# Optimization experiments

Hardware: AMD Instinct MI355X
Metric: run time of the kernel (lower is better)

Reference implementation:

```python
import jax, jax.numpy as jnp
import numpy as np

N = 50000      # nodes
E = 800000     # edges (avg degree 16)
D = 64         # hidden_dim = heads * per-head channels
H = 4          # heads
C = D // H     # per-head channels
EDIM = 16      # edge feature dim
L = 3          # num_layers
NEG_SLOPE = 0.2


def setup_inputs() -> dict:
    key = jax.random.key(0)
    ks = jax.random.split(key, 11)
    s = 0.1
    return {
        "x": jax.random.normal(ks[0], (N, D), dtype=jnp.float32),
        "edge_index": jax.random.randint(ks[1], (2, E), 0, N, dtype=jnp.int32),
        "edge_attr": jax.random.normal(ks[2], (E, EDIM), dtype=jnp.float32),
        # stacked per-layer GATv2 parameters (all layers have in=out=D)
        "Wl": jax.random.normal(ks[3], (L, D, D), dtype=jnp.float32) * s,
        "bl": jnp.zeros((L, D), dtype=jnp.float32),
        "Wr": jax.random.normal(ks[4], (L, D, D), dtype=jnp.float32) * s,
        "br": jnp.zeros((L, D), dtype=jnp.float32),
        "We": jax.random.normal(ks[5], (L, EDIM, D), dtype=jnp.float32) * s,
        "att": jax.random.normal(ks[6], (L, H, C), dtype=jnp.float32) * s,
        "bias": jnp.zeros((L, D), dtype=jnp.float32),
    }


def _gatv2_layer(x, src, dst, edge_attr, Wl, bl, Wr, br, We, att, bias):
    # x: [N, D] -> out: [N, D] (concat of H heads of C channels)
    xl = (x @ Wl + bl).reshape(N, H, C)          # source transform (message value)
    xr = (x @ Wr + br).reshape(N, H, C)          # target transform
    ef = (edge_attr @ We).reshape(E, H, C)       # edge feature transform
    m = jax.nn.leaky_relu(xl[src] + xr[dst] + ef, NEG_SLOPE)  # [E, H, C]
    score = jnp.einsum('ehc,hc->eh', m, att)     # [E, H]
    # segment softmax over incoming edges of each target node
    smax = jax.ops.segment_max(score, dst, num_segments=N)   # [N, H]
    ex = jnp.exp(score - smax[dst])                          # [E, H]
    denom = jax.ops.segment_sum(ex, dst, num_segments=N)     # [N, H]
    alpha = ex / denom[dst]                                  # [E, H]
    out = jax.ops.segment_sum(alpha[:, :, None] * xl[src], dst, num_segments=N)
    return out.reshape(N, D) + bias


def reference(x, edge_index, edge_attr, Wl, bl, Wr, br, We, att, bias):
    src, dst = edge_index[0], edge_index[1]
    h = x
    for l in range(L):
        h = _gatv2_layer(h, src, dst, edge_attr,
                         Wl[l], bl[l], Wr[l], br[l], We[l], att[l], bias[l])
        h = jax.nn.relu(h)
    return h
```

## Files before the change

### kernel.cpp

```cpp
#include <hip/hip_runtime.h>
#include <cfloat>

#define NEG_SLOPE 0.2f

__global__ __launch_bounds__(256) void zero_kernel(int* __restrict__ counts,
                                                   int* __restrict__ cursor, int n) {
    int gid = blockIdx.x * 256 + threadIdx.x;
    if (gid < n) { counts[gid] = 0; cursor[gid] = 0; }
}

__global__ __launch_bounds__(256) void count_kernel(const int* __restrict__ dst,
                                                    int* __restrict__ counts, int E) {
    int e = blockIdx.x * 256 + threadIdx.x;
    if (e < E) atomicAdd(&counts[dst[e]], 1);
}

__global__ __launch_bounds__(256) void scan_bsums_kernel(const int* __restrict__ counts,
                                                         int* __restrict__ bsums, int N) {
    int t = threadIdx.x;
    int base = blockIdx.x * 1024 + t * 4;
    int s = 0;
    #pragma unroll
    for (int i = 0; i < 4; ++i) { int idx = base + i; if (idx < N) s += counts[idx]; }
    #pragma unroll
    for (int d = 1; d < 64; d <<= 1) s += __shfl_xor(s, d);
    __shared__ int ws[4];
    if ((t & 63) == 0) ws[t >> 6] = s;
    __syncthreads();
    if (t == 0) bsums[blockIdx.x] = ws[0] + ws[1] + ws[2] + ws[3];
}

__global__ __launch_bounds__(64) void scan_bscan_kernel(int* __restrict__ bsums, int NB) {
    int t = threadIdx.x;
    int v = (t < NB) ? bsums[t] : 0;
    int x = v;
    #pragma unroll
    for (int d = 1; d < 64; d <<= 1) {
        int y = __shfl_up(x, d);
        if (t >= d) x += y;
    }
    if (t < NB) bsums[t] = x - v;
}

__global__ __launch_bounds__(256) void scan_final_kernel(const int* __restrict__ counts,
                                                         const int* __restrict__ bsums,
                                                         int* __restrict__ offs, int N) {
    int t = threadIdx.x, lane = t & 63, w = t >> 6;
    int base = blockIdx.x * 1024 + t * 4;
    int v[4]; int s = 0;
    #pragma unroll
    for (int i = 0; i < 4; ++i) { int idx = base + i; v[i] = (idx < N) ? counts[idx] : 0; s += v[i]; }
    int x = s;
    #pragma unroll
    for (int d = 1; d < 64; d <<= 1) {
        int y = __shfl_up(x, d);
        if (lane >= d) x += y;
    }
    __shared__ int wtot[4];
    if (lane == 63) wtot[w] = x;
    __syncthreads();
    int wexc = 0;
    for (int i = 0; i < w; ++i) wexc += wtot[i];
    int run = (x - s) + wexc + bsums[blockIdx.x];
    #pragma unroll
    for (int i = 0; i < 4; ++i) {
        int idx = base + i;
        run += v[i];
        if (idx < N) offs[idx + 1] = run;
    }
    if (blockIdx.x == 0 && t == 0) offs[0] = 0;
}

__global__ __launch_bounds__(256) void scatter_kernel(
    const int* __restrict__ src, const int* __restrict__ dst,
    const int* __restrict__ offs, int* __restrict__ cursor,
    int* __restrict__ csr_src, int* __restrict__ csr_dst,
    int* __restrict__ csr_eid, int E) {
    int e = blockIdx.x * 256 + threadIdx.x;
    if (e >= E) return;
    int d = dst[e];
    int pos = offs[d] + atomicAdd(&cursor[d], 1);
    csr_src[pos] = src[e];
    csr_dst[pos] = d;
    csr_eid[pos] = e;
}

__global__ __launch_bounds__(256) void sort_segments_kernel(
    int* __restrict__ csr_src, int* __restrict__ csr_eid,
    const int* __restrict__ offs, int N)
{
    int t = threadIdx.x;
    int lane = t & 63;
    int node = blockIdx.x * 4 + (t >> 6);
    if (node >= N) return;
    int off = offs[node];
    int deg = offs[node + 1] - off;
    if (deg <= 1) return;
    if (deg <= 64) {
        int key = 0x7FFFFFFF, val = 0;
        if (lane < deg) { key = csr_eid[off + lane]; val = csr_src[off + lane]; }
        int rank = 0;
        #pragma unroll
        for (int i = 0; i < 64; ++i) {
            int ki = __shfl(key, i);
            if (ki < key) rank++;
        }
        if (lane < deg) { csr_eid[off + rank] = key; csr_src[off + rank] = val; }
    } else if (lane == 0) {
        for (int a = 1; a < deg; ++a) {
            int k = csr_eid[off + a], v = csr_src[off + a];
            int b = a - 1;
            while (b >= 0 && csr_eid[off + b] > k) {
                csr_eid[off + b + 1] = csr_eid[off + b];
                csr_src[off + b + 1] = csr_src[off + b];
                b--;
            }
            csr_eid[off + b + 1] = k;
            csr_src[off + b + 1] = v;
        }
    }
}

#define XSTRIDE 68
__global__ __launch_bounds__(256) void node_gemm_kernel(
    const float* __restrict__ hin,
    const float* __restrict__ Wl, const float* __restrict__ bl,
    const float* __restrict__ Wr, const float* __restrict__ br,
    float* __restrict__ xl, float* __restrict__ xr, int nrows)
{
    __shared__ float sWl[4096];
    __shared__ float sWr[4096];
    __shared__ float sX[64 * XSTRIDE];
    int t = threadIdx.x;
    {
        float4* dl = (float4*)sWl; const float4* sl = (const float4*)Wl;
        float4* dr = (float4*)sWr; const float4* sr = (const float4*)Wr;
        for (int i = t; i < 1024; i += 256) { dl[i] = sl[i]; dr[i] = sr[i]; }
    }
    int row0 = blockIdx.x * 64;
    for (int i = t; i < 1024; i += 256) {
        int rr = i >> 4;
        int cc = (i & 15) << 2;
        int row = row0 + rr;
        float4 v = make_float4(0.f, 0.f, 0.f, 0.f);
        if (row < nrows) v = *(const float4*)(hin + (size_t)row * 64 + cc);
        *(float4*)(&sX[rr * XSTRIDE + cc]) = v;
    }
    __syncthreads();

    int lane = t & 63;
    int w = t >> 6;
    int rs = lane >> 4;
    int c4 = lane & 15;
    float4 bl4 = *(const float4*)(bl + c4 * 4);
    float4 br4 = *(const float4*)(br + c4 * 4);

    #pragma unroll
    for (int g = 0; g < 4; ++g) {
        int rloc = w * 16 + g * 4 + rs;
        int row = row0 + rloc;
        float4 al = {0.f, 0.f, 0.f, 0.f};
        float4 ar = {0.f, 0.f, 0.f, 0.f};
        const float* xrow = &sX[rloc * XSTRIDE];
        #pragma unroll 4
        for (int k = 0; k < 64; ++k) {
            float xk = xrow[k];
            float4 wl4 = *(const float4*)(&sWl[k * 64 + c4 * 4]);
            float4 wr4 = *(const float4*)(&sWr[k * 64 + c4 * 4]);
            al.x += xk * wl4.x; al.y += xk * wl4.y;
            al.z += xk * wl4.z; al.w += xk * wl4.w;
            ar.x += xk * wr4.x; ar.y += xk * wr4.y;
            ar.z += xk * wr4.z; ar.w += xk * wr4.w;
        }
        if (row < nrows) {
            float4 ol, orr;
            ol.x = al.x + bl4.x; ol.y = al.y + bl4.y;
            ol.z = al.z + bl4.z; ol.w = al.w + bl4.w;
            orr.x = ar.x + br4.x; orr.y = ar.y + br4.y;
            orr.z = ar.z + br4.z; orr.w = ar.w + br4.w;
            *(float4*)(xl + (size_t)row * 64 + c4 * 4) = ol;
            *(float4*)(xr + (size_t)row * 64 + c4 * 4) = orr;
        }
    }
}

__global__ __launch_bounds__(256) void edge_score_kernel(
    const float* __restrict__ xl, const float* __restrict__ xr,
    const float* __restrict__ ea,
    const int* __restrict__ csr_src, const int* __restrict__ csr_dst,
    const int* __restrict__ csr_eid,
    const float* __restrict__ We, const float* __restrict__ att,
    float* __restrict__ score_csr, int E)
{
    __shared__ float sWe[1024];
    __shared__ float sAtt[64];
    int t = threadIdx.x;
    for (int i = t; i < 1024; i += 256) sWe[i] = We[i];
    if (t < 64) sAtt[t] = att[t];
    __syncthreads();
    int gid = blockIdx.x * 256 + t;
    int pos = gid >> 2, h = gid & 3;
    if (pos >= E) return;
    int s = csr_src[pos], d = csr_dst[pos], eid = csr_eid[pos];
    const float4* eap = (const float4*)(ea + (size_t)eid * 16);
    float4 a0 = eap[0], a1 = eap[1], a2 = eap[2], a3 = eap[3];
    float av[16] = {a0.x, a0.y, a0.z, a0.w, a1.x, a1.y, a1.z, a1.w,
                    a2.x, a2.y, a2.z, a2.w, a3.x, a3.y, a3.z, a3.w};
    const float4* xls = (const float4*)(xl + (size_t)s * 64 + h * 16);
    const float4* xrd = (const float4*)(xr + (size_t)d * 64 + h * 16);
    float4 vl0 = xls[0], vl1 = xls[1], vl2 = xls[2], vl3 = xls[3];
    float4 vr0 = xrd[0], vr1 = xrd[1], vr2 = xrd[2], vr3 = xrd[3];

    float ef[16];
    #pragma unroll
    for (int c = 0; c < 16; ++c) ef[c] = 0.f;
    #pragma unroll
    for (int k = 0; k < 16; ++k) {
        float a = av[k];
        const float* wrow = &sWe[k * 64 + h * 16];
        #pragma unroll
        for (int c = 0; c < 16; ++c) ef[c] += a * wrow[c];
    }

    float lv[16] = {vl0.x, vl0.y, vl0.z, vl0.w, vl1.x, vl1.y, vl1.z, vl1.w,
                    vl2.x, vl2.y, vl2.z, vl2.w, vl3.x, vl3.y, vl3.z, vl3.w};
    float rv[16] = {vr0.x, vr0.y, vr0.z, vr0.w, vr1.x, vr1.y, vr1.z, vr1.w,
                    vr2.x, vr2.y, vr2.z, vr2.w, vr3.x, vr3.y, vr3.z, vr3.w};
    float sc0 = 0.f, sc1 = 0.f, sc2 = 0.f, sc3 = 0.f;
    #pragma unroll
    for (int c = 0; c < 16; c += 4) {
        float m0 = lv[c] + rv[c] + ef[c];
        float m1 = lv[c+1] + rv[c+1] + ef[c+1];
        float m2 = lv[c+2] + rv[c+2] + ef[c+2];
        float m3 = lv[c+3] + rv[c+3] + ef[c+3];
        m0 = (m0 >= 0.f) ? m0 : NEG_SLOPE * m0;
        m1 = (m1 >= 0.f) ? m1 : NEG_SLOPE * m1;
        m2 = (m2 >= 0.f) ? m2 : NEG_SLOPE * m2;
        m3 = (m3 >= 0.f) ? m3 : NEG_SLOPE * m3;
        sc0 += m0 * sAtt[h * 16 + c];
        sc1 += m1 * sAtt[h * 16 + c + 1];
        sc2 += m2 * sAtt[h * 16 + c + 2];
        sc3 += m3 * sAtt[h * 16 + c + 3];
    }
    score_csr[gid] = (sc0 + sc1) + (sc2 + sc3);
}

__global__ __launch_bounds__(256) void node_pass_kernel(
    const float* __restrict__ score_csr, const float* __restrict__ xl,
    const int* __restrict__ csr_src,
    const int* __restrict__ offs, const float* __restrict__ bias,
    float* __restrict__ hout, int N)
{
    int t = threadIdx.x;
    int lane = t & 63;
    int node = blockIdx.x * 4 + (t >> 6);
    if (node >= N) return;
    int eg = lane >> 4;
    int k  = lane & 15;
    int h  = k >> 2;
    int off = offs[node];
    int deg = offs[node + 1] - off;

    if (deg == 0) {
        if (eg == 0) {
            float4 b = *(const float4*)(bias + k * 4);
            float4 o;
            o.x = fmaxf(b.x, 0.f); o.y = fmaxf(b.y, 0.f);
            o.z = fmaxf(b.z, 0.f); o.w = fmaxf(b.w, 0.f);
            *(float4*)(hout + (size_t)node * 64 + k * 4) = o;
        }
        return;
    }

    float mx = -FLT_MAX;
    for (int j0 = 0; j0 < deg; j0 += 4) {
        int j = j0 + eg;
        if (j < deg) {
            float sc = score_csr[(size_t)(off + j) * 4 + h];
            mx = fmaxf(mx, sc);
        }
    }
    mx = fmaxf(mx, __shfl_xor(mx, 16));
    mx = fmaxf(mx, __shfl_xor(mx, 32));

    float4 acc = {0.f, 0.f, 0.f, 0.f};
    float sSum = 0.f;
    for (int j0 = 0; j0 < deg; j0 += 4) {
        int j = j0 + eg;
        int jj = (j < deg) ? j : deg - 1;
        int pos = off + jj;
        int s = csr_src[pos];
        float sc = score_csr[(size_t)pos * 4 + h];
        float ex = (j < deg) ? __expf(sc - mx) : 0.f;
        float4 v = *(const float4*)(xl + (size_t)s * 64 + k * 4);
        acc.x += ex * v.x; acc.y += ex * v.y;
        acc.z += ex * v.z; acc.w += ex * v.w;
        sSum += ex;
    }

    acc.x += __shfl_xor(acc.x, 16); acc.y += __shfl_xor(acc.y, 16);
    acc.z += __shfl_xor(acc.z, 16); acc.w += __shfl_xor(acc.w, 16);
    sSum  += __shfl_xor(sSum, 16);
    acc.x += __shfl_xor(acc.x, 32); acc.y += __shfl_xor(acc.y, 32);
    acc.z += __shfl_xor(acc.z, 32); acc.w += __shfl_xor(acc.w, 32);
    sSum  += __shfl_xor(sSum, 32);

    if (eg == 0) {
        float inv = 1.f / sSum;
        float4 b = *(const float4*)(bias + k * 4);
        float4 o;
        o.x = fmaxf(acc.x * inv + b.x, 0.f);
        o.y = fmaxf(acc.y * inv + b.y, 0.f);
        o.z = fmaxf(acc.z * inv + b.z, 0.f);
        o.w = fmaxf(acc.w * inv + b.w, 0.f);
        *(float4*)(hout + (size_t)node * 64 + k * 4) = o;
    }
}

extern "C" void kernel_launch(void* const* d_in, const int* in_sizes, int n_in,
                              void* d_out, int out_size, void* d_ws, size_t ws_size,
                              hipStream_t stream) {
    const float* x    = (const float*)d_in[0];
    const int*   eidx = (const int*)d_in[1];
    const float* ea   = (const float*)d_in[2];
    const float* Wl   = (const float*)d_in[3];
    const float* bl   = (const float*)d_in[4];
    const float* Wr   = (const float*)d_in[5];
    const float* br   = (const float*)d_in[6];
    const float* We   = (const float*)d_in[7];
    const float* att  = (const float*)d_in[8];
    const float* bias = (const float*)d_in[9];
    float* out = (float*)d_out;

    const int N = in_sizes[0] / 64;
    const int E = in_sizes[1] / 2;
    const int* src = eidx;
    const int* dst = eidx + E;

    float* ws = (float*)d_ws;
    float* xl      = ws;
    float* xr      = xl + (size_t)N * 64;
    float* score   = xr + (size_t)N * 64;
    float* h_tmp   = score + (size_t)E * 4;
    int* counts    = (int*)(h_tmp + (size_t)N * 64);
    int* cursor    = counts + N;
    int* offs      = cursor + N;
    int* csr_src   = offs + N + 1;
    int* csr_dst   = csr_src + E;
    int* csr_eid   = csr_dst + E;
    int* bsums     = csr_eid + E;

    dim3 blk(256);
    int g_n    = (N + 255) / 256;
    int g_e    = (E + 255) / 256;
    int g_eh   = (E * 4 + 255) / 256;
    int g_gemm = (N + 63) / 64;
    int g_node = (N + 3) / 4;
    int NB     = (N + 1023) / 1024;

    zero_kernel<<<g_n, blk, 0, stream>>>(counts, cursor, N);
    count_kernel<<<g_e, blk, 0, stream>>>(dst, counts, E);
    scan_bsums_kernel<<<NB, blk, 0, stream>>>(counts, bsums, N);
    scan_bscan_kernel<<<1, 64, 0, stream>>>(bsums, NB);
    scan_final_kernel<<<NB, blk, 0, stream>>>(counts, bsums, offs, N);
    scatter_kernel<<<g_e, blk, 0, stream>>>(src, dst, offs, cursor,
                                            csr_src, csr_dst, csr_eid, E);
    sort_segments_kernel<<<g_node, blk, 0, stream>>>(csr_src, csr_eid, offs, N);

    const float* hin = x;
    for (int l = 0; l < 3; ++l) {
        float* hout = (l == 2) ? out : h_tmp;
        node_gemm_kernel<<<g_gemm, blk, 0, stream>>>(hin, Wl + (size_t)l * 4096, bl + l * 64,
                                                     Wr + (size_t)l * 4096, br + l * 64, xl, xr, N);
        edge_score_kernel<<<g_eh, blk, 0, stream>>>(xl, xr, ea, csr_src, csr_dst, csr_eid,
                                                    We + (size_t)l * 1024, att + l * 64,
                                                    score, E);
        node_pass_kernel<<<g_node, blk, 0, stream>>>(score, xl, csr_src, offs,
                                                     bias + l * 64, hout, N);
        hin = hout;
    }
}
```

Baseline: 512.5 us.

## Fuse edge scoring and softmax aggregation into one online-softmax node kernel

Replaces the separate per-edge score kernel and per-node softmax/aggregation kernel with a single kernel in which each wavefront handles one destination node. It computes edge features, scores and an online softmax over incoming edges, so the score buffer is never written or read back. It also packs the CSR src and edge-id arrays into one int2 array and drops csr_dst. The trade-off is a serial per-edge loop within each wavefront, with a shuffle reduction and exp calls on every edge, which gives less parallelism than the old edge-parallel scoring.

Measured after the change: 625.9 us. +22.1%, slower.

```diff
diff --git a/kernel.cpp b/kernel.cpp
--- a/kernel.cpp
+++ b/kernel.cpp
@@ -74,20 +74,16 @@
 __global__ __launch_bounds__(256) void scatter_kernel(
     const int* __restrict__ src, const int* __restrict__ dst,
     const int* __restrict__ offs, int* __restrict__ cursor,
-    int* __restrict__ csr_src, int* __restrict__ csr_dst,
-    int* __restrict__ csr_eid, int E) {
+    int2* __restrict__ csr_se, int E) {
     int e = blockIdx.x * 256 + threadIdx.x;
     if (e >= E) return;
     int d = dst[e];
     int pos = offs[d] + atomicAdd(&cursor[d], 1);
-    csr_src[pos] = src[e];
-    csr_dst[pos] = d;
-    csr_eid[pos] = e;
+    csr_se[pos] = make_int2(src[e], e);
 }
 
 __global__ __launch_bounds__(256) void sort_segments_kernel(
-    int* __restrict__ csr_src, int* __restrict__ csr_eid,
-    const int* __restrict__ offs, int N)
+    int2* __restrict__ csr_se, const int* __restrict__ offs, int N)
 {
     int t = threadIdx.x;
     int lane = t & 63;
@@ -98,25 +94,23 @@
     if (deg <= 1) return;
     if (deg <= 64) {
         int key = 0x7FFFFFFF, val = 0;
-        if (lane < deg) { key = csr_eid[off + lane]; val = csr_src[off + lane]; }
+        if (lane < deg) { int2 se = csr_se[off + lane]; key = se.y; val = se.x; }
         int rank = 0;
         #pragma unroll
         for (int i = 0; i < 64; ++i) {
             int ki = __shfl(key, i);
             if (ki < key) rank++;
         }
-        if (lane < deg) { csr_eid[off + rank] = key; csr_src[off + rank] = val; }
+        if (lane < deg) csr_se[off + rank] = make_int2(val, key);
     } else if (lane == 0) {
         for (int a = 1; a < deg; ++a) {
-            int k = csr_eid[off + a], v = csr_src[off + a];
+            int2 kv = csr_se[off + a];
             int b = a - 1;
-            while (b >= 0 && csr_eid[off + b] > k) {
-                csr_eid[off + b + 1] = csr_eid[off + b];
-                csr_src[off + b + 1] = csr_src[off + b];
+            while (b >= 0 && csr_se[off + b].y > kv.y) {
+                csr_se[off + b + 1] = csr_se[off + b];
                 b--;
             }
-            csr_eid[off + b + 1] = k;
-            csr_src[off + b + 1] = v;
+            csr_se[off + b + 1] = kv;
         }
     }
 }
@@ -184,137 +178,56 @@
     }
 }
 
-__global__ __launch_bounds__(256) void edge_score_kernel(
+__global__ __launch_bounds__(256) void fused_attn_kernel(
     const float* __restrict__ xl, const float* __restrict__ xr,
     const float* __restrict__ ea,
-    const int* __restrict__ csr_src, const int* __restrict__ csr_dst,
-    const int* __restrict__ csr_eid,
+    const int2* __restrict__ csr_se, const int* __restrict__ offs,
     const float* __restrict__ We, const float* __restrict__ att,
-    float* __restrict__ score_csr, int E)
-{
-    __shared__ float sWe[1024];
-    __shared__ float sAtt[64];
-    int t = threadIdx.x;
-    for (int i = t; i < 1024; i += 256) sWe[i] = We[i];
-    if (t < 64) sAtt[t] = att[t];
-    __syncthreads();
-    int gid = blockIdx.x * 256 + t;
-    int pos = gid >> 2, h = gid & 3;
-    if (pos >= E) return;
-    int s = csr_src[pos], d = csr_dst[pos], eid = csr_eid[pos];
-    const float4* eap = (const float4*)(ea + (size_t)eid * 16);
-    float4 a0 = eap[0], a1 = eap[1], a2 = eap[2], a3 = eap[3];
-    float av[16] = {a0.x, a0.y, a0.z, a0.w, a1.x, a1.y, a1.z, a1.w,
-                    a2.x, a2.y, a2.z, a2.w, a3.x, a3.y, a3.z, a3.w};
-    const float4* xls = (const float4*)(xl + (size_t)s * 64 + h * 16);
-    const float4* xrd = (const float4*)(xr + (size_t)d * 64 + h * 16);
-    float4 vl0 = xls[0], vl1 = xls[1], vl2 = xls[2], vl3 = xls[3];
-    float4 vr0 = xrd[0], vr1 = xrd[1], vr2 = xrd[2], vr3 = xrd[3];
-
-    float ef[16];
-    #pragma unroll
-    for (int c = 0; c < 16; ++c) ef[c] = 0.f;
-    #pragma unroll
-    for (int k = 0; k < 16; ++k) {
-        float a = av[k];
-        const float* wrow = &sWe[k * 64 + h * 16];
-        #pragma unroll
-        for (int c = 0; c < 16; ++c) ef[c] += a * wrow[c];
-    }
-
-    float lv[16] = {vl0.x, vl0.y, vl0.z, vl0.w, vl1.x, vl1.y, vl1.z, vl1.w,
-                    vl2.x, vl2.y, vl2.z, vl2.w, vl3.x, vl3.y, vl3.z, vl3.w};
-    float rv[16] = {vr0.x, vr0.y, vr0.z, vr0.w, vr1.x, vr1.y, vr1.z, vr1.w,
-                    vr2.x, vr2.y, vr2.z, vr2.w, vr3.x, vr3.y, vr3.z, vr3.w};
-    float sc0 = 0.f, sc1 = 0.f, sc2 = 0.f, sc3 = 0.f;
-    #pragma unroll
-    for (int c = 0; c < 16; c += 4) {
-        float m0 = lv[c] + rv[c] + ef[c];
-        float m1 = lv[c+1] + rv[c+1] + ef[c+1];
-        float m2 = lv[c+2] + rv[c+2] + ef[c+2];
-        float m3 = lv[c+3] + rv[c+3] + ef[c+3];
-        m0 = (m0 >= 0.f) ? m0 : NEG_SLOPE * m0;
-        m1 = (m1 >= 0.f) ? m1 : NEG_SLOPE * m1;
-        m2 = (m2 >= 0.f) ? m2 : NEG_SLOPE * m2;
-        m3 = (m3 >= 0.f) ? m3 : NEG_SLOPE * m3;
-        sc0 += m0 * sAtt[h * 16 + c];
-        sc1 += m1 * sAtt[h * 16 + c + 1];
-        sc2 += m2 * sAtt[h * 16 + c + 2];
-        sc3 += m3 * sAtt[h * 16 + c + 3];
-    }
-    score_csr[gid] = (sc0 + sc1) + (sc2 + sc3);
-}
-
-__global__ __launch_bounds__(256) void node_pass_kernel(
-    const float* __restrict__ score_csr, const float* __restrict__ xl,
-    const int* __restrict__ csr_src,
-    const int* __restrict__ offs, const float* __restrict__ bias,
-    float* __restrict__ hout, int N)
+    const float* __restrict__ bias, float* __restrict__ hout, int N)
 {
     int t = threadIdx.x;
     int lane = t & 63;
     int node = blockIdx.x * 4 + (t >> 6);
     if (node >= N) return;
-    int eg = lane >> 4;
-    int k  = lane & 15;
-    int h  = k >> 2;
+
+    float wv[16];
+    #pragma unroll
+    for (int k = 0; k < 16; ++k) wv[k] = We[k * 64 + lane];
+    float attc = att[lane];
+    float bc   = bias[lane];
+    float xrc  = xr[(size_t)node * 64 + lane];
+
     int off = offs[node];
     int deg = offs[node + 1] - off;
 
-    if (deg == 0) {
-        if (eg == 0) {
-            float4 b = *(const float4*)(bias + k * 4);
-            float4 o;
-            o.x = fmaxf(b.x, 0.f); o.y = fmaxf(b.y, 0.f);
-            o.z = fmaxf(b.z, 0.f); o.w = fmaxf(b.w, 0.f);
-            *(float4*)(hout + (size_t)node * 64 + k * 4) = o;
-        }
-        return;
-    }
-
-    float mx = -FLT_MAX;
-    for (int j0 = 0; j0 < deg; j0 += 4) {
-        int j = j0 + eg;
-        if (j < deg) {
-            float sc = score_csr[(size_t)(off + j) * 4 + h];
-            mx = fmaxf(mx, sc);
-        }
-    }
-    mx = fmaxf(mx, __shfl_xor(mx, 16));
-    mx = fmaxf(mx, __shfl_xor(mx, 32));
-
-    float4 acc = {0.f, 0.f, 0.f, 0.f};
-    float sSum = 0.f;
-    for (int j0 = 0; j0 < deg; j0 += 4) {
-        int j = j0 + eg;
-        int jj = (j < deg) ? j : deg - 1;
-        int pos = off + jj;
-        int s = csr_src[pos];
-        float sc = score_csr[(size_t)pos * 4 + h];
-        float ex = (j < deg) ? __expf(sc - mx) : 0.f;
-        float4 v = *(const float4*)(xl + (size_t)s * 64 + k * 4);
-        acc.x += ex * v.x; acc.y += ex * v.y;
-        acc.z += ex * v.z; acc.w += ex * v.w;
-        sSum += ex;
-    }
-
-    acc.x += __shfl_xor(acc.x, 16); acc.y += __shfl_xor(acc.y, 16);
-    acc.z += __shfl_xor(acc.z, 16); acc.w += __shfl_xor(acc.w, 16);
-    sSum  += __shfl_xor(sSum, 16);
-    acc.x += __shfl_xor(acc.x, 32); acc.y += __shfl_xor(acc.y, 32);
-    acc.z += __shfl_xor(acc.z, 32); acc.w += __shfl_xor(acc.w, 32);
-    sSum  += __shfl_xor(sSum, 32);
-
-    if (eg == 0) {
-        float inv = 1.f / sSum;
-        float4 b = *(const float4*)(bias + k * 4);
-        float4 o;
-        o.x = fmaxf(acc.x * inv + b.x, 0.f);
-        o.y = fmaxf(acc.y * inv + b.y, 0.f);
-        o.z = fmaxf(acc.z * inv + b.z, 0.f);
-        o.w = fmaxf(acc.w * inv + b.w, 0.f);
-        *(float4*)(hout + (size_t)node * 64 + k * 4) = o;
-    }
+    float m = -FLT_MAX, s = 0.f, acc = 0.f;
+    for (int j = 0; j < deg; ++j) {
+        int2 se = csr_se[off + j];
+        const float4* ap = (const float4*)(ea + (size_t)se.y * 16);
+        float4 a0 = ap[0], a1 = ap[1], a2 = ap[2], a3 = ap[3];
+        float xlc = xl[(size_t)se.x * 64 + lane];
+        float ef = a0.x * wv[0]  + a0.y * wv[1]  + a0.z * wv[2]  + a0.w * wv[3]
+                 + a1.x * wv[4]  + a1.y * wv[5]  + a1.z * wv[6]  + a1.w * wv[7]
+                 + a2.x * wv[8]  + a2.y * wv[9]  + a2.z * wv[10] + a2.w * wv[11]
+                 + a3.x * wv[12] + a3.y * wv[13] + a3.z * wv[14] + a3.w * wv[15];
+        float mm = xlc + xrc + ef;
+        mm = (mm >= 0.f) ? mm : NEG_SLOPE * mm;
+        float sc = mm * attc;
+        sc += __shfl_xor(sc, 1);
+        sc += __shfl_xor(sc, 2);
+        sc += __shfl_xor(sc, 4);
+        sc += __shfl_xor(sc, 8);
+        float nm = fmaxf(m, sc);
+        float scale = __expf(m - nm);
+        float p = __expf(sc - nm);
+        s   = s * scale + p;
+        acc = acc * scale + p * xlc;
+        m = nm;
+    }
+
+    float v = (deg > 0) ? (acc / s) : 0.f;
+    v += bc;
+    hout[(size_t)node * 64 + lane] = fmaxf(v, 0.f);
 }
 
 extern "C" void kernel_launch(void* const* d_in, const int* in_sizes, int n_in,
@@ -340,20 +253,16 @@
     float* ws = (float*)d_ws;
     float* xl      = ws;
     float* xr      = xl + (size_t)N * 64;
-    float* score   = xr + (size_t)N * 64;
-    float* h_tmp   = score + (size_t)E * 4;
+    float* h_tmp   = xr + (size_t)N * 64;
     int* counts    = (int*)(h_tmp + (size_t)N * 64);
     int* cursor    = counts + N;
     int* offs      = cursor + N;
-    int* csr_src   = offs + N + 1;
-    int* csr_dst   = csr_src + E;
-    int* csr_eid   = csr_dst + E;
-    int* bsums     = csr_eid + E;
+    int* bsums     = offs + N + 1;
+    int2* csr_se   = (int2*)(bsums + 64);
 
     dim3 blk(256);
     int g_n    = (N + 255) / 256;
     int g_e    = (E + 255) / 256;
-    int g_eh   = (E * 4 + 255) / 256;
     int g_gemm = (N + 63) / 64;
     int g_node = (N + 3) / 4;
     int NB     = (N + 1023) / 1024;
@@ -363,20 +272,17 @@
     scan_bsums_kernel<<<NB, blk, 0, stream>>>(counts, bsums, N);
     scan_bscan_kernel<<<1, 64, 0, stream>>>(bsums, NB);
     scan_final_kernel<<<NB, blk, 0, stream>>>(counts, bsums, offs, N);
-    scatter_kernel<<<g_e, blk, 0, stream>>>(src, dst, offs, cursor,
-                                            csr_src, csr_dst, csr_eid, E);
-    sort_segments_kernel<<<g_node, blk, 0, stream>>>(csr_src, csr_eid, offs, N);
+    scatter_kernel<<<g_e, blk, 0, stream>>>(src, dst, offs, cursor, csr_se, E);
+    sort_segments_kernel<<<g_node, blk, 0, stream>>>(csr_se, offs, N);
 
     const float* hin = x;
     for (int l = 0; l < 3; ++l) {
         float* hout = (l == 2) ? out : h_tmp;
         node_gemm_kernel<<<g_gemm, blk, 0, stream>>>(hin, Wl + (size_t)l * 4096, bl + l * 64,
                                                      Wr + (size_t)l * 4096, br + l * 64, xl, xr, N);
-        edge_score_kernel<<<g_eh, blk, 0, stream>>>(xl, xr, ea, csr_src, csr_dst, csr_eid,
-                                                    We + (size_t)l * 1024, att + l * 64,
-                                                    score, E);
-        node_pass_kernel<<<g_node, blk, 0, stream>>>(score, xl, csr_src, offs,
-                                                     bias + l * 64, hout, N);
+        fused_attn_kernel<<<g_node, blk, 0, stream>>>(xl, xr, ea, csr_se, offs,
+                                                      We + (size_t)l * 1024, att + l * 64,
+                                                      bias + l * 64, hout, N);
         hin = hout;
     }
 }
```

## Pack CSR edge arrays into int4 and pre-permute edge attributes into CSR order

Applied to the files above, without the earlier changes.

Merges the separate src, dst and edge-id CSR arrays into one int4 array per edge, so each edge's indices are fetched with a single 16-byte load. Adds a one-time kernel that copies edge_attr into CSR order, so the three per-layer edge-score passes read edge features contiguously instead of gathering them by edge id. The permuted copy is used only when the workspace is large enough; otherwise the code falls back to the gather. The cost is an extra 51 MB copy pass and a larger CSR footprint (padding lane), and node_pass now loads a 16-byte struct where it previously loaded a 4-byte int.

Result: slower. 527.1 us (+2.9%).

```diff
diff --git a/kernel.cpp b/kernel.cpp
--- a/kernel.cpp
+++ b/kernel.cpp
@@ -74,20 +74,16 @@
 __global__ __launch_bounds__(256) void scatter_kernel(
     const int* __restrict__ src, const int* __restrict__ dst,
     const int* __restrict__ offs, int* __restrict__ cursor,
-    int* __restrict__ csr_src, int* __restrict__ csr_dst,
-    int* __restrict__ csr_eid, int E) {
+    int4* __restrict__ csr, int E) {
     int e = blockIdx.x * 256 + threadIdx.x;
     if (e >= E) return;
     int d = dst[e];
     int pos = offs[d] + atomicAdd(&cursor[d], 1);
-    csr_src[pos] = src[e];
-    csr_dst[pos] = d;
-    csr_eid[pos] = e;
+    csr[pos] = make_int4(src[e], d, e, 0);
 }
 
 __global__ __launch_bounds__(256) void sort_segments_kernel(
-    int* __restrict__ csr_src, int* __restrict__ csr_eid,
-    const int* __restrict__ offs, int N)
+    int4* __restrict__ csr, const int* __restrict__ offs, int N)
 {
     int t = threadIdx.x;
     int lane = t & 63;
@@ -97,28 +93,38 @@
     int deg = offs[node + 1] - off;
     if (deg <= 1) return;
     if (deg <= 64) {
-        int key = 0x7FFFFFFF, val = 0;
-        if (lane < deg) { key = csr_eid[off + lane]; val = csr_src[off + lane]; }
+        int key = 0x7FFFFFFF; int4 kv = make_int4(0, 0, 0, 0);
+        if (lane < deg) { kv = csr[off + lane]; key = kv.z; }
         int rank = 0;
         #pragma unroll
         for (int i = 0; i < 64; ++i) {
             int ki = __shfl(key, i);
             if (ki < key) rank++;
         }
-        if (lane < deg) { csr_eid[off + rank] = key; csr_src[off + rank] = val; }
+        if (lane < deg) csr[off + rank] = kv;
     } else if (lane == 0) {
         for (int a = 1; a < deg; ++a) {
-            int k = csr_eid[off + a], v = csr_src[off + a];
+            int4 kv = csr[off + a];
             int b = a - 1;
-            while (b >= 0 && csr_eid[off + b] > k) {
-                csr_eid[off + b + 1] = csr_eid[off + b];
-                csr_src[off + b + 1] = csr_src[off + b];
+            while (b >= 0 && csr[off + b].z > kv.z) {
+                csr[off + b + 1] = csr[off + b];
                 b--;
             }
-            csr_eid[off + b + 1] = k;
-            csr_src[off + b + 1] = v;
-        }
-    }
+            csr[off + b + 1] = kv;
+        }
+    }
+}
+
+__global__ __launch_bounds__(256) void eaperm_kernel(
+    const float* __restrict__ ea, const int4* __restrict__ csr,
+    float* __restrict__ eaperm, int E)
+{
+    int gid = blockIdx.x * 256 + threadIdx.x;
+    int pos = gid >> 2, q = gid & 3;
+    if (pos >= E) return;
+    int eid = csr[pos].z;
+    *(float4*)(eaperm + (size_t)pos * 16 + q * 4) =
+        *(const float4*)(ea + (size_t)eid * 16 + q * 4);
 }
 
 #define XSTRIDE 68
@@ -186,9 +192,8 @@
 
 __global__ __launch_bounds__(256) void edge_score_kernel(
     const float* __restrict__ xl, const float* __restrict__ xr,
-    const float* __restrict__ ea,
-    const int* __restrict__ csr_src, const int* __restrict__ csr_dst,
-    const int* __restrict__ csr_eid,
+    const float* __restrict__ ea, const float* __restrict__ eaperm, int use_perm,
+    const int4* __restrict__ csr,
     const float* __restrict__ We, const float* __restrict__ att,
     float* __restrict__ score_csr, int E)
 {
@@ -201,8 +206,11 @@
     int gid = blockIdx.x * 256 + t;
     int pos = gid >> 2, h = gid & 3;
     if (pos >= E) return;
-    int s = csr_src[pos], d = csr_dst[pos], eid = csr_eid[pos];
-    const float4* eap = (const float4*)(ea + (size_t)eid * 16);
+    int4 se = csr[pos];
+    int s = se.x, d = se.y;
+    const float4* eap = use_perm
+        ? (const float4*)(eaperm + (size_t)pos * 16)
+        : (const float4*)(ea + (size_t)se.z * 16);
     float4 a0 = eap[0], a1 = eap[1], a2 = eap[2], a3 = eap[3];
     float av[16] = {a0.x, a0.y, a0.z, a0.w, a1.x, a1.y, a1.z, a1.w,
                     a2.x, a2.y, a2.z, a2.w, a3.x, a3.y, a3.z, a3.w};
@@ -247,7 +255,7 @@
 
 __global__ __launch_bounds__(256) void node_pass_kernel(
     const float* __restrict__ score_csr, const float* __restrict__ xl,
-    const int* __restrict__ csr_src,
+    const int4* __restrict__ csr,
     const int* __restrict__ offs, const float* __restrict__ bias,
     float* __restrict__ hout, int N)
 {
@@ -289,7 +297,7 @@
         int j = j0 + eg;
         int jj = (j < deg) ? j : deg - 1;
         int pos = off + jj;
-        int s = csr_src[pos];
+        int s = csr[pos].x;
         float sc = score_csr[(size_t)pos * 4 + h];
         float ex = (j < deg) ? __expf(sc - mx) : 0.f;
         float4 v = *(const float4*)(xl + (size_t)s * 64 + k * 4);
@@ -345,10 +353,15 @@
     int* counts    = (int*)(h_tmp + (size_t)N * 64);
     int* cursor    = counts + N;
     int* offs      = cursor + N;
-    int* csr_src   = offs + N + 1;
-    int* csr_dst   = csr_src + E;
-    int* csr_eid   = csr_dst + E;
-    int* bsums     = csr_eid + E;
+    int* bsums     = offs + N + 1;
+    uintptr_t p    = (uintptr_t)(bsums + 64);
+    p = (p + 15) & ~(uintptr_t)15;
+    int4* csr      = (int4*)p;
+    float* eaperm  = (float*)(csr + E);
+
+    size_t need_base = (uintptr_t)(eaperm) - (uintptr_t)d_ws;
+    size_t need_perm = need_base + (size_t)E * 16 * sizeof(float);
+    int use_perm = (ws_size >= need_perm) ? 1 : 0;
 
     dim3 blk(256);
     int g_n    = (N + 255) / 256;
@@ -363,19 +376,20 @@
     scan_bsums_kernel<<<NB, blk, 0, stream>>>(counts, bsums, N);
     scan_bscan_kernel<<<1, 64, 0, stream>>>(bsums, NB);
     scan_final_kernel<<<NB, blk, 0, stream>>>(counts, bsums, offs, N);
-    scatter_kernel<<<g_e, blk, 0, stream>>>(src, dst, offs, cursor,
-                                            csr_src, csr_dst, csr_eid, E);
-    sort_segments_kernel<<<g_node, blk, 0, stream>>>(csr_src, csr_eid, offs, N);
+    scatter_kernel<<<g_e, blk, 0, stream>>>(src, dst, offs, cursor, csr, E);
+    sort_segments_kernel<<<g_node, blk, 0, stream>>>(csr, offs, N);
+    if (use_perm)
+        eaperm_kernel<<<g_eh, blk, 0, stream>>>(ea, csr, eaperm, E);
 
     const float* hin = x;
     for (int l = 0; l < 3; ++l) {
         float* hout = (l == 2) ? out : h_tmp;
         node_gemm_kernel<<<g_gemm, blk, 0, stream>>>(hin, Wl + (size_t)l * 4096, bl + l * 64,
                                                      Wr + (size_t)l * 4096, br + l * 64, xl, xr, N);
-        edge_score_kernel<<<g_eh, blk, 0, stream>>>(xl, xr, ea, csr_src, csr_dst, csr_eid,
+        edge_score_kernel<<<g_eh, blk, 0, stream>>>(xl, xr, ea, eaperm, use_perm, csr,
                                                     We + (size_t)l * 1024, att + l * 64,
                                                     score, E);
-        node_pass_kernel<<<g_node, blk, 0, stream>>>(score, xl, csr_src, offs,
+        node_pass_kernel<<<g_node, blk, 0, stream>>>(score, xl, csr, offs,
                                                      bias + l * 64, hout, N);
         hin = hout;
     }
```
